# Optimization experiments

Hardware: AMD Instinct MI355X
Metric: run time of the kernel (lower is better)

The kernel has to match this reference:

```python
import jax, jax.numpy as jnp
import numpy as np

N = 50000   # nodes
E = 600000  # edges (before self-loops)
D = 128     # input_dim
H = 128     # hidden_dim
NEG_SLOPE = 0.2  # GATConv default


def setup_inputs() -> dict:
    key = jax.random.key(0)
    ks = jax.random.split(key, 16)
    inp = {
        "x": jax.random.normal(ks[0], (N, D), jnp.float32),
        "edge_index": jax.random.randint(ks[1], (2, E), 0, N, dtype=jnp.int64),
        "edge_attr": jax.random.normal(ks[2], (E, 1), jnp.float32),
    }
    # GATConv params per layer: lin W [H,in] (no bias), att_src/att_dst [H],
    # lin_edge We [H,1] (no bias), att_edge [H], final bias b [H]
    def mk(k, shape, fan_in):
        return jax.random.normal(k, shape, jnp.float32) / np.sqrt(fan_in)
    ins = [D, H]
    ki = 3
    for i in range(2):
        cin = ins[i]
        inp[f"W{i}"] = mk(ks[ki], (H, cin), cin); ki += 1
        inp[f"att_src{i}"] = mk(ks[ki], (H,), H); ki += 1
        inp[f"att_dst{i}"] = mk(ks[ki], (H,), H); ki += 1
        inp[f"We{i}"] = mk(ks[ki], (H, 1), 1); ki += 1
        inp[f"att_e{i}"] = mk(ks[ki], (H,), H); ki += 1
        inp[f"b{i}"] = jnp.zeros((H,), jnp.float32)
    return inp


def _gat_forward(x, edge_index, edge_attr, params):
    # add self loops; self-loop edge_attr = mean of edge_attr (fill_value='mean')
    src = jnp.concatenate([edge_index[0], jnp.arange(N, dtype=edge_index.dtype)])
    dst = jnp.concatenate([edge_index[1], jnp.arange(N, dtype=edge_index.dtype)])
    ea = jnp.concatenate(
        [edge_attr, jnp.broadcast_to(edge_attr.mean(0, keepdims=True), (N, 1))], 0
    )  # [E+N, 1]

    def gat_layer(h, W, b, a_s, a_d, We, a_e):
        hp = h @ W.T                                   # [N, H]
        e_lin = ea @ We.T                              # [E+N, H]
        alpha = (hp @ a_s)[src] + (hp @ a_d)[dst] + e_lin @ a_e  # [E+N]
        alpha = jax.nn.leaky_relu(alpha, NEG_SLOPE)
        # segment softmax over destination nodes
        m = jax.ops.segment_max(alpha, dst, num_segments=N)
        m = jnp.where(jnp.isfinite(m), m, 0.0)
        w = jnp.exp(alpha - m[dst])
        denom = jax.ops.segment_sum(w, dst, num_segments=N)
        w = w / (denom[dst] + 1e-16)
        out = jax.ops.segment_sum(hp[src] * w[:, None], dst, num_segments=N)
        return out + b

    layer_outs = [x]
    h = x
    for i in range(2):
        h = jax.nn.relu(
            gat_layer(h, params[f"W{i}"], params[f"b{i}"], params[f"att_src{i}"],
                      params[f"att_dst{i}"], params[f"We{i}"], params[f"att_e{i}"])
        )
        layer_outs.append(h)
    return jnp.concatenate(layer_outs, axis=-1)  # JK 'cat': [N, D + 2H]


def reference(x, edge_index, edge_attr,
              W0, att_src0, att_dst0, We0, att_e0, b0,
              W1, att_src1, att_dst1, We1, att_e1, b1):
    params = {
        "W0": W0, "att_src0": att_src0, "att_dst0": att_dst0, "We0": We0,
        "att_e0": att_e0, "b0": b0,
        "W1": W1, "att_src1": att_src1, "att_dst1": att_dst1, "We1": We1,
        "att_e1": att_e1, "b1": b1,
    }
    return _gat_forward(x, edge_index, edge_attr, params)
```

## Files before the change

kernel.cpp:

```cpp
#include <hip/hip_runtime.h>
#include <hip/hip_fp16.h>
#include <math.h>

#define N_NODES 50000
#define N_EDGES 600000
#define TOT (N_EDGES + N_NODES)
#define HD 128
#define OUTW 384
#define NEG_SLOPE 0.2f

#define BM 128
#define GB 391
#define AGB 3125
#define NCHUNK 49
#define FILLB 256

#define XBLK 6250
#define WBLK 64
#define DBLK 2540
#define SBLK 64


typedef _Float16 h2_t __attribute__((ext_vector_type(2)));

static __device__ __forceinline__ float fdot2f(h2_t a, h2_t b, float c){
#if __has_builtin(__builtin_amdgcn_fdot2)
  return __builtin_amdgcn_fdot2(a, b, c, false);
#else
  return fmaf((float)a[0], (float)b[0], fmaf((float)a[1], (float)b[1], c));
#endif
}

static __device__ __forceinline__ int load_edge(const void* ei, int is64, long long off){
  return is64 ? (int)((const long long*)ei)[off] : ((const int*)ei)[off];
}

__global__ __launch_bounds__(256) void conv_kernel(const float* __restrict__ x,
                                                   __half* __restrict__ x16,
                                                   float* __restrict__ out,
                                                   const float* __restrict__ W0, const float* __restrict__ W1,
                                                   __half2* __restrict__ Wt0, __half2* __restrict__ Wt1,
                                                   const void* ei, int* deg,
                                                   int* __restrict__ src32, int* __restrict__ dst32,
                                                   const float* __restrict__ eattr, float* scal,
                                                   const float* __restrict__ We0, const float* __restrict__ ae0,
                                                   const float* __restrict__ We1, const float* __restrict__ ae1){
  int b = blockIdx.x;
  int t = threadIdx.x;
  if (b < XBLK){
    int idx = b * 256 + t;
    int n = idx >> 5, c4 = idx & 31;
    float4 v = ((const float4*)x)[idx];
    *(float4*)&out[(size_t)n * OUTW + c4 * 4] = v;
    float2 pk;
    ((__half2*)&pk)[0] = __floats2half2_rn(v.x, v.y);
    ((__half2*)&pk)[1] = __floats2half2_rn(v.z, v.w);
    *(float2*)&x16[(size_t)idx * 4] = pk;
  } else if (b < XBLK + WBLK){
    int e = (b - XBLK) * 256 + t;
    const float* W = (e < 8192) ? W0 : W1;
    __half2* Wt = (e < 8192) ? Wt0 : Wt1;
    int i = e & 8191;
    int n = i & 127, k2 = i >> 7;
    float a = W[n * HD + 2 * k2];
    float c = W[n * HD + 2 * k2 + 1];
    Wt[k2 * 128 + n] = __floats2half2_rn(a, c);
  } else if (b < XBLK + WBLK + DBLK){
    __shared__ int s_is64;
    if (t < 64){
      long long v = ((const long long*)ei)[t];
      unsigned long long bad = __ballot(v < 0 || v >= N_NODES);
      if (t == 0) s_is64 = (bad == 0ull) ? 1 : 0;
    }
    __syncthreads();
    int is64 = s_is64;
    int e = (b - XBLK - WBLK) * 256 + t;
    if (e < TOT){
      int d;
      if (e < N_EDGES){
        int s = load_edge(ei, is64, e);
        d = load_edge(ei, is64, (long long)N_EDGES + e);
        src32[e] = s;
        dst32[e] = d;
      } else {
        d = e - N_EDGES;
      }
      atomicAdd(&deg[d], 1);
    }
  } else if (b < XBLK + WBLK + DBLK + SBLK){
    int gtid = (b - XBLK - WBLK - DBLK) * 256 + t;
    float s = 0.f;
    for (int i = gtid; i < N_EDGES; i += SBLK * 256) s += eattr[i];
    #pragma unroll
    for (int o = 32; o > 0; o >>= 1) s += __shfl_down(s, o, 64);
    if ((t & 63) == 0) atomicAdd(&scal[0], s);
  } else {
    int w = t >> 6, lane = t & 63;
    if (w == 1){
      float s = We0[lane] * ae0[lane] + We0[lane + 64] * ae0[lane + 64];
      #pragma unroll
      for (int o = 32; o > 0; o >>= 1) s += __shfl_down(s, o, 64);
      if (lane == 0) scal[1] = s;
    } else if (w == 2){
      float s = We1[lane] * ae1[lane] + We1[lane + 64] * ae1[lane + 64];
      #pragma unroll
      for (int o = 32; o > 0; o >>= 1) s += __shfl_down(s, o, 64);
      if (lane == 0) scal[2] = s;
    }
  }
}


__global__ __launch_bounds__(256) void scan_chunk_kernel(const int* __restrict__ deg,
                                                         int* __restrict__ rowstart,
                                                         int* __restrict__ chunksums){
  __shared__ int sums[256];
  int t = threadIdx.x;
  int base = blockIdx.x * 1024 + t * 4;
  int v[4];
  #pragma unroll
  for (int i = 0; i < 4; i++) v[i] = (base + i < N_NODES) ? deg[base + i] : 0;
  int tsum = v[0] + v[1] + v[2] + v[3];
  sums[t] = tsum;
  __syncthreads();
  for (int off = 1; off < 256; off <<= 1){
    int add = (t >= off) ? sums[t - off] : 0;
    __syncthreads();
    sums[t] += add;
    __syncthreads();
  }
  int run = sums[t] - tsum;
  #pragma unroll
  for (int i = 0; i < 4; i++){
    if (base + i < N_NODES) rowstart[base + i] = run;
    run += v[i];
  }
  if (t == 255) chunksums[blockIdx.x] = sums[255];
}

__global__ __launch_bounds__(256) void add_off_kernel(int* rowstart, int* rowcur,
                                                      const int* __restrict__ chunksums){
  __shared__ int soff;
  int t = threadIdx.x;
  if (t < 64){
    int v = (t < blockIdx.x) ? chunksums[t] : 0;
    for (int o = 32; o > 0; o >>= 1) v += __shfl_down(v, o, 64);
    if (t == 0) soff = v;
  }
  __syncthreads();
  int off = soff;
  int base = blockIdx.x * 1024 + t * 4;
  #pragma unroll
  for (int i = 0; i < 4; i++){
    if (base + i < N_NODES){
      int v = rowstart[base + i] + off;
      rowstart[base + i] = v;
      rowcur[base + i] = v;
    }
  }
}

__device__ __forceinline__ void gemm_tile512(int tb, int t, __half2* As2, __half2* Wh2,
                                             const __half* __restrict__ hin,
                                             const __half2* __restrict__ Wt,
                                             __half* __restrict__ hp_h,
                                             const float* __restrict__ as_,
                                             const float* __restrict__ ad_,
                                             float* __restrict__ ssrc,
                                             float* __restrict__ sdst){
  int tx = t & 15;
  int ty = t >> 4;
  int rb = tb * BM;

  {
    const float4* src = (const float4*)Wt;
    float4* dst = (float4*)Wh2;
    #pragma unroll
    for (int p = 0; p < 4; p++) dst[t + p * 512] = src[t + p * 512];
  }
  #pragma unroll
  for (int p = 0; p < 4; p++){
    int idx = t + p * 512;
    int row = idx >> 4, c8 = idx & 15;
    int gr = rb + row; if (gr >= N_NODES) gr = N_NODES - 1;
    float4 v = *(const float4*)&hin[(size_t)gr * HD + c8 * 8];
    __half2* hv = (__half2*)&v;
    #pragma unroll
    for (int q = 0; q < 4; q++) As2[(4 * c8 + q) * 128 + row] = hv[q];
  }
  __syncthreads();

  float acc[4][8];
  #pragma unroll
  for (int i = 0; i < 4; i++)
    #pragma unroll
    for (int j = 0; j < 8; j++) acc[i][j] = 0.f;

  #pragma unroll 4
  for (int k2 = 0; k2 < 64; k2++){
    float4 ar0 = *(const float4*)&As2[k2 * 128 + ty * 4];
    float4 wr0 = *(const float4*)&Wh2[k2 * 128 + tx * 4];
    float4 wr1 = *(const float4*)&Wh2[k2 * 128 + 64 + tx * 4];
    const h2_t* av = (const h2_t*)&ar0;
    const h2_t* wv0 = (const h2_t*)&wr0;
    const h2_t* wv1 = (const h2_t*)&wr1;
    #pragma unroll
    for (int i = 0; i < 4; i++){
      h2_t ai = av[i];
      #pragma unroll
      for (int j = 0; j < 4; j++){
        acc[i][j]     = fdot2f(ai, wv0[j], acc[i][j]);
        acc[i][j + 4] = fdot2f(ai, wv1[j], acc[i][j + 4]);
      }
    }
  }

  #pragma unroll
  for (int i = 0; i < 4; i++){
    int r = rb + ty * 4 + i;
    if (r < N_NODES){
      float2 s0, s1;
      ((__half2*)&s0)[0] = __floats2half2_rn(acc[i][0], acc[i][1]);
      ((__half2*)&s0)[1] = __floats2half2_rn(acc[i][2], acc[i][3]);
      ((__half2*)&s1)[0] = __floats2half2_rn(acc[i][4], acc[i][5]);
      ((__half2*)&s1)[1] = __floats2half2_rn(acc[i][6], acc[i][7]);
      *(float2*)&hp_h[(size_t)r * HD + tx * 4]      = s0;
      *(float2*)&hp_h[(size_t)r * HD + 64 + tx * 4] = s1;
    }
  }

  float as_v[8], ad_v[8];
  #pragma unroll
  for (int j = 0; j < 4; j++){
    as_v[j]     = as_[tx * 4 + j];      ad_v[j]     = ad_[tx * 4 + j];
    as_v[j + 4] = as_[64 + tx * 4 + j]; ad_v[j + 4] = ad_[64 + tx * 4 + j];
  }
  #pragma unroll
  for (int i = 0; i < 4; i++){
    float ps = 0.f, pd = 0.f;
    #pragma unroll
    for (int j = 0; j < 8; j++){
      ps = fmaf(acc[i][j], as_v[j], ps);
      pd = fmaf(acc[i][j], ad_v[j], pd);
    }
    #pragma unroll
    for (int off = 8; off > 0; off >>= 1){
      ps += __shfl_down(ps, off, 16);
      pd += __shfl_down(pd, off, 16);
    }
    int r = rb + ty * 4 + i;
    if (tx == 0 && r < N_NODES){ ssrc[r] = ps; sdst[r] = pd; }
  }
}

__global__ __launch_bounds__(512, 4) void fillgemm_kernel(const __half* __restrict__ hin,
                                                          const __half2* __restrict__ Wt,
                                                          __half* __restrict__ hp_h,
                                                          const float* __restrict__ as_,
                                                          const float* __restrict__ ad_,
                                                          float* __restrict__ ssrc,
                                                          float* __restrict__ sdst,
                                                          const int* __restrict__ src32,
                                                          const int* __restrict__ dst32,
                                                          int* rowcur, int2* __restrict__ csr){
  __shared__ __align__(16) __half2 As2[64 * 128];
  __shared__ __align__(16) __half2 Wh2[64 * 128];
  int b = blockIdx.x;
  if (b < GB){
    gemm_tile512(b, threadIdx.x, As2, Wh2, hin, Wt, hp_h, as_, ad_, ssrc, sdst);
  } else {
    int gtid = (b - GB) * 512 + threadIdx.x;
    for (int e = gtid; e < TOT; e += FILLB * 512){
      int s, d;
      if (e < N_EDGES){
        s = src32[e];
        d = dst32[e];
      } else {
        s = d = e - N_EDGES;
      }
      int pos = atomicAdd(&rowcur[d], 1);
      csr[pos] = make_int2(s, e);
    }
  }
}

__global__ __launch_bounds__(512, 4) void gemm_kernel(const __half* __restrict__ hin,
                                                      const __half2* __restrict__ Wt,
                                                      __half* __restrict__ hp_h,
                                                      const float* __restrict__ as_,
                                                      const float* __restrict__ ad_,
                                                      float* __restrict__ ssrc,
                                                      float* __restrict__ sdst){
  __shared__ __align__(16) __half2 As2[64 * 128];
  __shared__ __align__(16) __half2 Wh2[64 * 128];
  gemm_tile512(blockIdx.x, threadIdx.x, As2, Wh2, hin, Wt, hp_h, as_, ad_, ssrc, sdst);
}

__global__ __launch_bounds__(256) void agg_kernel(const int* __restrict__ rowstart,
                                                  const int2* __restrict__ csr,
                                                  const float* __restrict__ eattr,
                                                  const float* __restrict__ ssrc,
                                                  const float* __restrict__ sdst,
                                                  const float* __restrict__ scal, int which,
                                                  const __half* __restrict__ hp_h,
                                                  const float* __restrict__ bias,
                                                  __half* __restrict__ hnext,
                                                  float* __restrict__ out, int outoff){
  int sub  = threadIdx.x >> 4;
  int lane = threadIdx.x & 15;
  int n = blockIdx.x * 16 + sub;
  int s0 = rowstart[n];
  int s1 = (n + 1 < N_NODES) ? rowstart[n + 1] : TOT;
  float sd = sdst[n];
  float ce = scal[1 + which];
  float mean_ea = scal[0] * (1.0f / (float)N_EDGES);
  float4 bA = *(const float4*)&bias[lane * 8];
  float4 bB = *(const float4*)&bias[lane * 8 + 4];
  const float4* hb = (const float4*)hp_h;

  float a0 = 0.f, a1 = 0.f, a2 = 0.f, a3 = 0.f;
  float a4 = 0.f, a5 = 0.f, a6 = 0.f, a7 = 0.f;
  float sum = 0.f;

#define EW(se) ({ float eav = ((se).y < N_EDGES) ? eattr[(se).y] : mean_ea;       \
    float al = ssrc[(se).x] + sd + eav * ce;                                      \
    al = (al >= 0.f) ? al : NEG_SLOPE * al;                                       \
    expf(al); })

#define ACC8(r, p) { const __half2* hh = (const __half2*)&(r); float2 f;         \
    f = __half22float2(hh[0]); a0 = fmaf(p, f.x, a0); a1 = fmaf(p, f.y, a1);     \
    f = __half22float2(hh[1]); a2 = fmaf(p, f.x, a2); a3 = fmaf(p, f.y, a3);     \
    f = __half22float2(hh[2]); a4 = fmaf(p, f.x, a4); a5 = fmaf(p, f.y, a5);     \
    f = __half22float2(hh[3]); a6 = fmaf(p, f.x, a6); a7 = fmaf(p, f.y, a7); }

  int i = s0;
  for (; i + 8 <= s1; i += 8){
    int2 se[8]; float4 r[8];
    #pragma unroll
    for (int u = 0; u < 8; u++) se[u] = csr[i + u];
    #pragma unroll
    for (int u = 0; u < 8; u++) r[u] = hb[(size_t)se[u].x * 16 + lane];
    #pragma unroll
    for (int u = 0; u < 8; u++){
      float p = EW(se[u]);
      sum += p;
      ACC8(r[u], p);
    }
  }
  for (; i < s1; i++){
    int2 se = csr[i];
    float4 r = hb[(size_t)se.x * 16 + lane];
    float p = EW(se);
    sum += p;
    ACC8(r, p);
  }
#undef ACC8
#undef EW

  float inv = 1.0f / (sum + 1e-16f);
  float v0 = fmaf(a0, inv, bA.x); v0 = v0 > 0.f ? v0 : 0.f;
  float v1 = fmaf(a1, inv, bA.y); v1 = v1 > 0.f ? v1 : 0.f;
  float v2 = fmaf(a2, inv, bA.z); v2 = v2 > 0.f ? v2 : 0.f;
  float v3 = fmaf(a3, inv, bA.w); v3 = v3 > 0.f ? v3 : 0.f;
  float v4 = fmaf(a4, inv, bB.x); v4 = v4 > 0.f ? v4 : 0.f;
  float v5 = fmaf(a5, inv, bB.y); v5 = v5 > 0.f ? v5 : 0.f;
  float v6 = fmaf(a6, inv, bB.z); v6 = v6 > 0.f ? v6 : 0.f;
  float v7 = fmaf(a7, inv, bB.w); v7 = v7 > 0.f ? v7 : 0.f;
  if (hnext){
    float4 pk;
    __half2* p2h = (__half2*)&pk;
    p2h[0] = __floats2half2_rn(v0, v1);
    p2h[1] = __floats2half2_rn(v2, v3);
    p2h[2] = __floats2half2_rn(v4, v5);
    p2h[3] = __floats2half2_rn(v6, v7);
    *(float4*)&hnext[(size_t)n * HD + lane * 8] = pk;
  }
  *(float4*)&out[(size_t)n * OUTW + outoff + lane * 8]     = make_float4(v0, v1, v2, v3);
  *(float4*)&out[(size_t)n * OUTW + outoff + lane * 8 + 4] = make_float4(v4, v5, v6, v7);
}


extern "C" void kernel_launch(void* const* d_in, const int* in_sizes, int n_in,
                              void* d_out, int out_size, void* d_ws, size_t ws_size,
                              hipStream_t stream){
  (void)in_sizes; (void)n_in; (void)out_size; (void)ws_size;
  const float* x    = (const float*)d_in[0];
  const void*  ei   = d_in[1];
  const float* eatt = (const float*)d_in[2];
  const float* W0   = (const float*)d_in[3];
  const float* as0  = (const float*)d_in[4];
  const float* ad0  = (const float*)d_in[5];
  const float* We0  = (const float*)d_in[6];
  const float* ae0  = (const float*)d_in[7];
  const float* b0   = (const float*)d_in[8];
  const float* W1   = (const float*)d_in[9];
  const float* as1  = (const float*)d_in[10];
  const float* ad1  = (const float*)d_in[11];
  const float* We1  = (const float*)d_in[12];
  const float* ae1  = (const float*)d_in[13];
  const float* b1   = (const float*)d_in[14];
  float* out = (float*)d_out;

  char* ws = (char*)d_ws;
  size_t off = 0;
  auto alloc = [&](size_t bytes) -> void* {
    void* p = ws + off;
    off += (bytes + 255) & ~(size_t)255;
    return p;
  };
  __half*   hp_h     = (__half*)  alloc((size_t)N_NODES * HD * 2);
  __half*   h1       = (__half*)  alloc((size_t)N_NODES * HD * 2);
  __half*   x16      = (__half*)  alloc((size_t)N_NODES * HD * 2);
  float*    ssrc     = (float*)   alloc((size_t)N_NODES * 4);
  float*    sdst     = (float*)   alloc((size_t)N_NODES * 4);
  int*      deg      = (int*)     alloc((size_t)N_NODES * 4);
  float*    scal     = (float*)   alloc(256);
  int*      rowstart = (int*)     alloc((size_t)N_NODES * 4);
  int*      rowcur   = (int*)     alloc((size_t)N_NODES * 4);
  int*      src32    = (int*)     alloc((size_t)N_EDGES * 4);
  int*      dst32    = (int*)     alloc((size_t)N_EDGES * 4);
  int2*     csr      = (int2*)    alloc((size_t)TOT * 8);
  __half2*  Wt0      = (__half2*) alloc((size_t)8192 * 4);
  __half2*  Wt1      = (__half2*) alloc((size_t)8192 * 4);
  int*      chunksums= (int*)     alloc(64 * 4);

  hipMemsetAsync(deg, 0, 200192 + 256, stream);

  conv_kernel<<<XBLK + WBLK + DBLK + SBLK + 1, 256, 0, stream>>>(
      x, x16, out, W0, W1, Wt0, Wt1, ei, deg, src32, dst32, eatt, scal,
      We0, ae0, We1, ae1);
  scan_chunk_kernel<<<NCHUNK, 256, 0, stream>>>(deg, rowstart, chunksums);
  add_off_kernel<<<NCHUNK, 256, 0, stream>>>(rowstart, rowcur, chunksums);

  fillgemm_kernel<<<GB + FILLB, 512, 0, stream>>>(x16, Wt0, hp_h, as0, ad0, ssrc, sdst,
                                                  src32, dst32, rowcur, csr);
  agg_kernel<<<AGB, 256, 0, stream>>>(rowstart, csr, eatt, ssrc, sdst, scal, 0,
                                      hp_h, b0, h1, out, 128);

  gemm_kernel<<<GB, 512, 0, stream>>>(h1, Wt1, hp_h, as1, ad1, ssrc, sdst);
  agg_kernel<<<AGB, 256, 0, stream>>>(rowstart, csr, eatt, ssrc, sdst, scal, 1,
                                      hp_h, b1, nullptr, out, 256);
}
```

Measured before the change: 311.2 us.

## Fuse x conversion into first GEMM and merge scan kernels via chunk flags

Drops the separate fp16 staging copy of x. The first-layer GEMM now reads fp32 x directly and converts it while loading the tile, and the copy of x into the output moves into extra blocks of the fill/GEMM kernel. The two-kernel prefix scan becomes a single kernel that publishes per-chunk sums through acquire/release flags and spins on earlier chunks. This removes a kernel launch and a full fp16 write and read of x. In exchange it relies on inter-block spin waiting, which assumes all 49 blocks are co-resident, and the GEMM now reads twice as many bytes for its A tile.

```diff
diff --git a/kernel.cpp b/kernel.cpp
--- a/kernel.cpp
+++ b/kernel.cpp
@@ -14,10 +14,10 @@
 #define AGB 3125
 #define NCHUNK 49
 #define FILLB 256
-
-#define XBLK 6250
+#define XC 1563
+
+#define DBLK 2540
 #define WBLK 64
-#define DBLK 2540
 #define SBLK 64
 
 
@@ -35,37 +35,16 @@
   return is64 ? (int)((const long long*)ei)[off] : ((const int*)ei)[off];
 }
 
-__global__ __launch_bounds__(256) void conv_kernel(const float* __restrict__ x,
-                                                   __half* __restrict__ x16,
-                                                   float* __restrict__ out,
+__global__ __launch_bounds__(256) void edge_kernel(const void* ei, int* deg,
+                                                   int* __restrict__ src32, int* __restrict__ dst32,
                                                    const float* __restrict__ W0, const float* __restrict__ W1,
                                                    __half2* __restrict__ Wt0, __half2* __restrict__ Wt1,
-                                                   const void* ei, int* deg,
-                                                   int* __restrict__ src32, int* __restrict__ dst32,
                                                    const float* __restrict__ eattr, float* scal,
                                                    const float* __restrict__ We0, const float* __restrict__ ae0,
                                                    const float* __restrict__ We1, const float* __restrict__ ae1){
   int b = blockIdx.x;
   int t = threadIdx.x;
-  if (b < XBLK){
-    int idx = b * 256 + t;
-    int n = idx >> 5, c4 = idx & 31;
-    float4 v = ((const float4*)x)[idx];
-    *(float4*)&out[(size_t)n * OUTW + c4 * 4] = v;
-    float2 pk;
-    ((__half2*)&pk)[0] = __floats2half2_rn(v.x, v.y);
-    ((__half2*)&pk)[1] = __floats2half2_rn(v.z, v.w);
-    *(float2*)&x16[(size_t)idx * 4] = pk;
-  } else if (b < XBLK + WBLK){
-    int e = (b - XBLK) * 256 + t;
-    const float* W = (e < 8192) ? W0 : W1;
-    __half2* Wt = (e < 8192) ? Wt0 : Wt1;
-    int i = e & 8191;
-    int n = i & 127, k2 = i >> 7;
-    float a = W[n * HD + 2 * k2];
-    float c = W[n * HD + 2 * k2 + 1];
-    Wt[k2 * 128 + n] = __floats2half2_rn(a, c);
-  } else if (b < XBLK + WBLK + DBLK){
+  if (b < DBLK){
     __shared__ int s_is64;
     if (t < 64){
       long long v = ((const long long*)ei)[t];
@@ -74,7 +53,7 @@
     }
     __syncthreads();
     int is64 = s_is64;
-    int e = (b - XBLK - WBLK) * 256 + t;
+    int e = b * 256 + t;
     if (e < TOT){
       int d;
       if (e < N_EDGES){
@@ -87,8 +66,17 @@
       }
       atomicAdd(&deg[d], 1);
     }
-  } else if (b < XBLK + WBLK + DBLK + SBLK){
-    int gtid = (b - XBLK - WBLK - DBLK) * 256 + t;
+  } else if (b < DBLK + WBLK){
+    int e = (b - DBLK) * 256 + t;
+    const float* W = (e < 8192) ? W0 : W1;
+    __half2* Wt = (e < 8192) ? Wt0 : Wt1;
+    int i = e & 8191;
+    int n = i & 127, k2 = i >> 7;
+    float a = W[n * HD + 2 * k2];
+    float c = W[n * HD + 2 * k2 + 1];
+    Wt[k2 * 128 + n] = __floats2half2_rn(a, c);
+  } else if (b < DBLK + WBLK + SBLK){
+    int gtid = (b - DBLK - WBLK) * 256 + t;
     float s = 0.f;
     for (int i = gtid; i < N_EDGES; i += SBLK * 256) s += eattr[i];
     #pragma unroll
@@ -110,13 +98,14 @@
   }
 }
 
-
-__global__ __launch_bounds__(256) void scan_chunk_kernel(const int* __restrict__ deg,
-                                                         int* __restrict__ rowstart,
-                                                         int* __restrict__ chunksums){
+__global__ __launch_bounds__(256) void scanfuse_kernel(const int* __restrict__ deg,
+                                                       int* __restrict__ rowstart,
+                                                       int* __restrict__ rowcur,
+                                                       int* chunkflag){
   __shared__ int sums[256];
-  int t = threadIdx.x;
-  int base = blockIdx.x * 1024 + t * 4;
+  __shared__ int soff;
+  int bid = blockIdx.x, t = threadIdx.x;
+  int base = bid * 1024 + t * 4;
   int v[4];
   #pragma unroll
   for (int i = 0; i < 4; i++) v[i] = (base + i < N_NODES) ? deg[base + i] : 0;
@@ -130,38 +119,41 @@
     __syncthreads();
   }
   int run = sums[t] - tsum;
-  #pragma unroll
-  for (int i = 0; i < 4; i++){
-    if (base + i < N_NODES) rowstart[base + i] = run;
-    run += v[i];
-  }
-  if (t == 255) chunksums[blockIdx.x] = sums[255];
-}
-
-__global__ __launch_bounds__(256) void add_off_kernel(int* rowstart, int* rowcur,
-                                                      const int* __restrict__ chunksums){
-  __shared__ int soff;
-  int t = threadIdx.x;
+
+  if (t == 255)
+    __hip_atomic_store(&chunkflag[bid], sums[255] + 1, __ATOMIC_RELEASE, __HIP_MEMORY_SCOPE_AGENT);
+
   if (t < 64){
-    int v = (t < blockIdx.x) ? chunksums[t] : 0;
-    for (int o = 32; o > 0; o >>= 1) v += __shfl_down(v, o, 64);
-    if (t == 0) soff = v;
+    int acc_ = 0;
+    for (int j = t; j < bid; j += 64){
+      int val;
+      long long spins = 0;
+      while ((val = __hip_atomic_load(&chunkflag[j], __ATOMIC_ACQUIRE, __HIP_MEMORY_SCOPE_AGENT)) == 0){
+        __builtin_amdgcn_s_sleep(1);
+        if (++spins > (1LL << 24)) break;
+      }
+      acc_ += val - 1;
+    }
+    #pragma unroll
+    for (int o = 32; o > 0; o >>= 1) acc_ += __shfl_down(acc_, o, 64);
+    if (t == 0) soff = acc_;
   }
   __syncthreads();
   int off = soff;
-  int base = blockIdx.x * 1024 + t * 4;
   #pragma unroll
   for (int i = 0; i < 4; i++){
     if (base + i < N_NODES){
-      int v = rowstart[base + i] + off;
-      rowstart[base + i] = v;
-      rowcur[base + i] = v;
-    }
-  }
-}
-
+      int r = run + off;
+      rowstart[base + i] = r;
+      rowcur[base + i] = r;
+    }
+    run += v[i];
+  }
+}
+
+template<bool F32>
 __device__ __forceinline__ void gemm_tile512(int tb, int t, __half2* As2, __half2* Wh2,
-                                             const __half* __restrict__ hin,
+                                             const void* __restrict__ hin,
                                              const __half2* __restrict__ Wt,
                                              __half* __restrict__ hp_h,
                                              const float* __restrict__ as_,
@@ -178,15 +170,29 @@
     #pragma unroll
     for (int p = 0; p < 4; p++) dst[t + p * 512] = src[t + p * 512];
   }
-  #pragma unroll
-  for (int p = 0; p < 4; p++){
-    int idx = t + p * 512;
-    int row = idx >> 4, c8 = idx & 15;
-    int gr = rb + row; if (gr >= N_NODES) gr = N_NODES - 1;
-    float4 v = *(const float4*)&hin[(size_t)gr * HD + c8 * 8];
-    __half2* hv = (__half2*)&v;
-    #pragma unroll
-    for (int q = 0; q < 4; q++) As2[(4 * c8 + q) * 128 + row] = hv[q];
+  if (F32){
+    const float* xin = (const float*)hin;
+    #pragma unroll
+    for (int p = 0; p < 8; p++){
+      int idx = t + p * 512;
+      int row = idx >> 5, c4 = idx & 31;
+      int gr = rb + row; if (gr >= N_NODES) gr = N_NODES - 1;
+      float4 v = *(const float4*)&xin[(size_t)gr * HD + c4 * 4];
+      As2[(2 * c4 + 0) * 128 + row] = __floats2half2_rn(v.x, v.y);
+      As2[(2 * c4 + 1) * 128 + row] = __floats2half2_rn(v.z, v.w);
+    }
+  } else {
+    const __half* hin16 = (const __half*)hin;
+    #pragma unroll
+    for (int p = 0; p < 4; p++){
+      int idx = t + p * 512;
+      int row = idx >> 4, c8 = idx & 15;
+      int gr = rb + row; if (gr >= N_NODES) gr = N_NODES - 1;
+      float4 v = *(const float4*)&hin16[(size_t)gr * HD + c8 * 8];
+      __half2* hv = (__half2*)&v;
+      #pragma unroll
+      for (int q = 0; q < 4; q++) As2[(4 * c8 + q) * 128 + row] = hv[q];
+    }
   }
   __syncthreads();
 
@@ -253,7 +259,7 @@
   }
 }
 
-__global__ __launch_bounds__(512, 4) void fillgemm_kernel(const __half* __restrict__ hin,
+__global__ __launch_bounds__(512, 4) void fillgemm_kernel(const float* __restrict__ x,
                                                           const __half2* __restrict__ Wt,
                                                           __half* __restrict__ hp_h,
                                                           const float* __restrict__ as_,
@@ -262,13 +268,14 @@
                                                           float* __restrict__ sdst,
                                                           const int* __restrict__ src32,
                                                           const int* __restrict__ dst32,
-                                                          int* rowcur, int2* __restrict__ csr){
+                                                          int* rowcur, int2* __restrict__ csr,
+                                                          float* __restrict__ out){
   __shared__ __align__(16) __half2 As2[64 * 128];
   __shared__ __align__(16) __half2 Wh2[64 * 128];
   int b = blockIdx.x;
   if (b < GB){
-    gemm_tile512(b, threadIdx.x, As2, Wh2, hin, Wt, hp_h, as_, ad_, ssrc, sdst);
-  } else {
+    gemm_tile512<true>(b, threadIdx.x, As2, Wh2, x, Wt, hp_h, as_, ad_, ssrc, sdst);
+  } else if (b < GB + FILLB){
     int gtid = (b - GB) * 512 + threadIdx.x;
     for (int e = gtid; e < TOT; e += FILLB * 512){
       int s, d;
@@ -281,6 +288,17 @@
       int pos = atomicAdd(&rowcur[d], 1);
       csr[pos] = make_int2(s, e);
     }
+  } else {
+    int base = (b - GB - FILLB) * 1024 + threadIdx.x;
+    #pragma unroll
+    for (int u = 0; u < 2; u++){
+      int idx = base + u * 512;
+      if (idx < N_NODES * HD / 4){
+        int n = idx >> 5, c4 = idx & 31;
+        float4 v = ((const float4*)x)[idx];
+        *(float4*)&out[(size_t)n * OUTW + c4 * 4] = v;
+      }
+    }
   }
 }
 
@@ -293,7 +311,7 @@
                                                       float* __restrict__ sdst){
   __shared__ __align__(16) __half2 As2[64 * 128];
   __shared__ __align__(16) __half2 Wh2[64 * 128];
-  gemm_tile512(blockIdx.x, threadIdx.x, As2, Wh2, hin, Wt, hp_h, as_, ad_, ssrc, sdst);
+  gemm_tile512<false>(blockIdx.x, threadIdx.x, As2, Wh2, hin, Wt, hp_h, as_, ad_, ssrc, sdst);
 }
 
 __global__ __launch_bounds__(256) void agg_kernel(const int* __restrict__ rowstart,
@@ -410,11 +428,11 @@
   };
   __half*   hp_h     = (__half*)  alloc((size_t)N_NODES * HD * 2);
   __half*   h1       = (__half*)  alloc((size_t)N_NODES * HD * 2);
-  __half*   x16      = (__half*)  alloc((size_t)N_NODES * HD * 2);
   float*    ssrc     = (float*)   alloc((size_t)N_NODES * 4);
   float*    sdst     = (float*)   alloc((size_t)N_NODES * 4);
   int*      deg      = (int*)     alloc((size_t)N_NODES * 4);
   float*    scal     = (float*)   alloc(256);
+  int*      chunkflag= (int*)     alloc(256);
   int*      rowstart = (int*)     alloc((size_t)N_NODES * 4);
   int*      rowcur   = (int*)     alloc((size_t)N_NODES * 4);
   int*      src32    = (int*)     alloc((size_t)N_EDGES * 4);
@@ -422,18 +440,15 @@
   int2*     csr      = (int2*)    alloc((size_t)TOT * 8);
   __half2*  Wt0      = (__half2*) alloc((size_t)8192 * 4);
   __half2*  Wt1      = (__half2*) alloc((size_t)8192 * 4);
-  int*      chunksums= (int*)     alloc(64 * 4);
-
-  hipMemsetAsync(deg, 0, 200192 + 256, stream);
-
-  conv_kernel<<<XBLK + WBLK + DBLK + SBLK + 1, 256, 0, stream>>>(
-      x, x16, out, W0, W1, Wt0, Wt1, ei, deg, src32, dst32, eatt, scal,
-      We0, ae0, We1, ae1);
-  scan_chunk_kernel<<<NCHUNK, 256, 0, stream>>>(deg, rowstart, chunksums);
-  add_off_kernel<<<NCHUNK, 256, 0, stream>>>(rowstart, rowcur, chunksums);
-
-  fillgemm_kernel<<<GB + FILLB, 512, 0, stream>>>(x16, Wt0, hp_h, as0, ad0, ssrc, sdst,
-                                                  src32, dst32, rowcur, csr);
+
+  hipMemsetAsync(deg, 0, 200192 + 256 + 256, stream);
+
+  edge_kernel<<<DBLK + WBLK + SBLK + 1, 256, 0, stream>>>(
+      ei, deg, src32, dst32, W0, W1, Wt0, Wt1, eatt, scal, We0, ae0, We1, ae1);
+  scanfuse_kernel<<<NCHUNK, 256, 0, stream>>>(deg, rowstart, rowcur, chunkflag);
+
+  fillgemm_kernel<<<GB + FILLB + XC, 512, 0, stream>>>(x, Wt0, hp_h, as0, ad0, ssrc, sdst,
+                                                       src32, dst32, rowcur, csr, out);
   agg_kernel<<<AGB, 256, 0, stream>>>(rowstart, csr, eatt, ssrc, sdst, scal, 0,
                                       hp_h, b0, h1, out, 128);
 
```

Measured after the change: 308.4 us. No clear change (-0.9%).
